# Performance work log

Hardware: AMD Instinct MI355X
Metric: run time of the kernel (lower is better)

Reference implementation:

```python
import jax, jax.numpy as jnp
import numpy as np

B, T, D = 64, 8192, 16   # batch, time, state dim
H = 128                  # recurr_size
HID = (256, 256)         # MLP hidden sizes
OUT = 1                  # output_dim
F = D + 1                # features + weight channel


def setup_inputs() -> dict:
    key = jax.random.key(0)
    ks = jax.random.split(key, 12)
    s = lambda k, shp: jax.random.normal(k, shp, jnp.float32) * 0.05
    return {
        "particles": jax.random.normal(ks[0], (B, T, D), jnp.float32),
        "weights": jax.random.uniform(ks[1], (B, T), jnp.float32),
        # GRU params: packed [r|z|n] gates; input dense has no bias (flax GRUCell),
        # hidden dense has bias.
        "Wi": s(ks[2], (F, 3 * H)),
        "Wh": s(ks[3], (H, 3 * H)),
        "bh": jnp.zeros((3 * H,), jnp.float32),
        # MLP decoder params
        "W1": s(ks[4], (H, HID[0])), "b1": jnp.zeros((HID[0],), jnp.float32),
        "W2": s(ks[5], (HID[0], HID[1])), "b2": jnp.zeros((HID[1],), jnp.float32),
        "W3": s(ks[6], (HID[1], OUT)), "b3": jnp.zeros((OUT,), jnp.float32),
        # log_std param, initialized with ones (init_log_std default)
        "log_std": jnp.ones((OUT,), jnp.float32),
    }


def _gru_last(inputs, Wi, Wh, bh):
    """Run GRU over time (axis 1 of [B,T,F]); return final hidden state [B,H].
    Equivalent to taking encoding at the last timestep."""
    h0 = jnp.zeros((inputs.shape[0], H), inputs.dtype)

    def step(h, x_t):  # x_t: [B,F]
        gi = x_t @ Wi              # [B,3H], no input bias (flax GRUCell)
        gh = h @ Wh + bh           # [B,3H]
        ir, iz, inn = jnp.split(gi, 3, axis=-1)
        hr, hz, hn = jnp.split(gh, 3, axis=-1)
        r = jax.nn.sigmoid(ir + hr)
        z = jax.nn.sigmoid(iz + hz)
        n = jnp.tanh(inn + r * hn)
        h_new = (1.0 - z) * n + z * h
        return h_new, None

    xs = jnp.swapaxes(inputs, 0, 1)  # [T,B,F]
    h_last, _ = jax.lax.scan(step, h0, xs)
    return h_last


def reference(particles, weights, Wi, Wh, bh, W1, b1, W2, b2, W3, b3, log_std):
    features = particles  # feature_fn = identity
    inputs = jnp.concatenate([features, weights[..., None]], axis=-1)  # [B,T,F]
    enc = _gru_last(inputs, Wi, Wh, bh)  # [B,H] == encoding at last timestep
    x = jax.nn.relu(enc @ W1 + b1)
    x = jax.nn.relu(x @ W2 + b2)
    mean = x @ W3 + b3  # [B,OUT]
    return mean, log_std
```

## Files before the change

kernel.cpp:

```cpp
#include <hip/hip_runtime.h>
#include <hip/hip_bf16.h>

#define B 64
#define T 8192
#define D 16
#define H 128
#define F 17
#define NTHREADS 512

typedef _Float16 half_t;
typedef _Float16 f16x8 __attribute__((ext_vector_type(8)));
typedef float f32x4 __attribute__((ext_vector_type(4)));

#define MFMA(a, b, c) __builtin_amdgcn_mfma_f32_16x16x32_f16((a), (b), (c), 0, 0, 0)

__device__ __forceinline__ float fast_rcp(float x) {
#if __has_builtin(__builtin_amdgcn_rcpf)
  return __builtin_amdgcn_rcpf(x);
#else
  return 1.0f / x;
#endif
}

#define GSTEP(RBUF, WBUF, tt, XV)                                          \
  do {                                                                     \
    const f16x8* hv8 = (const f16x8*)(RBUF);                               \
    f16x8 a0 = hv8[g16], a1 = hv8[4 + g16], a2 = hv8[8 + g16],             \
          a3 = hv8[12 + g16], a4 = hv8[16 + g16];                          \
    f32x4 ar = {b_r, b_r, b_r, b_r}, az = {b_z, b_z, b_z, b_z},            \
          an = {b_n, b_n, b_n, b_n}, ai = {0.f, 0.f, 0.f, 0.f};            \
    ar = MFMA(a0, wr0, ar); az = MFMA(a0, wz0, az); an = MFMA(a0, wn0, an);\
    ar = MFMA(a1, wr1, ar); az = MFMA(a1, wz1, az); an = MFMA(a1, wn1, an);\
    ar = MFMA(a2, wr2, ar); az = MFMA(a2, wz2, az); an = MFMA(a2, wn2, an);\
    ar = MFMA(a3, wr3, ar); az = MFMA(a3, wz3, az); an = MFMA(a3, wn3, an);\
    ar = MFMA(a4, wr4, ar); az = MFMA(a4, wz4, az); ai = MFMA(a4, wi4, ai);\
    float rr = fast_rcp(1.0f + __expf(-ar[0]));                            \
    float zz = fast_rcp(1.0f + __expf(-az[0]));                            \
    float pre = fmaf(rr, an[0], ai[0]);                                    \
    pre = fminf(fmaxf(pre, -15.0f), 15.0f);                                \
    float e2 = __expf(-2.0f * pre);                                        \
    float nn = (1.0f - e2) * fast_rcp(1.0f + e2);                          \
    hreg = fmaf(zz, hreg - nn, nn);                     \
    if (g16 == 0) (WBUF)[jj] = (half_t)hreg;                               \
    if (isx) { (WBUF)[H + tid] = (half_t)(XV);                             \
               XV = xload((tt) + 3 < T ? (tt) + 3 : T - 1); }              \
    __syncthreads();                                                       \
  } while (0)

__global__ __launch_bounds__(NTHREADS)
void policy_gru_kernel(const float* __restrict__ particles,
                       const float* __restrict__ weights,
                       const float* __restrict__ Wi, const float* __restrict__ Wh,
                       const float* __restrict__ bh,
                       const float* __restrict__ W1, const float* __restrict__ b1,
                       const float* __restrict__ W2, const float* __restrict__ b2,
                       const float* __restrict__ W3, const float* __restrict__ b3,
                       const float* __restrict__ log_std,
                       float* __restrict__ out)
{
  __shared__ __align__(16) half_t hbuf[2][160];
  __shared__ float sg[NTHREADS];
  __shared__ float red[8];

  const int tid = threadIdx.x;
  const int b   = blockIdx.x;
  const int l   = tid & 63;
  const int w   = tid >> 6;
  const int g16 = l >> 4;
  const int jn  = l & 15;
  const int jj  = w * 16 + jn;

  auto wload = [&](int gate, int s) -> f16x8 {
    f16x8 v;
    #pragma unroll
    for (int r = 0; r < 8; ++r) {
      const int k = s * 32 + g16 * 8 + r;
      float f = 0.0f;
      const int col = (gate == 0) ? jj : (gate == 1) ? 128 + jj : 256 + jj;
      if (gate <= 1) {
        if (k < 128) f = Wh[k * 384 + col];
        else if (k < 128 + F) f = Wi[(k - 128) * 384 + col];
      } else if (gate == 2) {
        if (k < 128) f = Wh[k * 384 + col];
      } else {
        if (k >= 128 && k < 128 + F) f = Wi[(k - 128) * 384 + col];
      }
      v[r] = (half_t)f;
    }
    return v;
  };
  const f16x8 wr0 = wload(0, 0), wr1 = wload(0, 1), wr2 = wload(0, 2),
              wr3 = wload(0, 3), wr4 = wload(0, 4);
  const f16x8 wz0 = wload(1, 0), wz1 = wload(1, 1), wz2 = wload(1, 2),
              wz3 = wload(1, 3), wz4 = wload(1, 4);
  const f16x8 wn0 = wload(2, 0), wn1 = wload(2, 1), wn2 = wload(2, 2),
              wn3 = wload(2, 3);
  const f16x8 wi4 = wload(3, 4);
  const float b_r = bh[jj], b_z = bh[128 + jj], b_n = bh[256 + jj];

  const bool isx = tid < F;
  auto xload = [&](int t) -> float {
    if (!isx) return 0.0f;
    if (tid < D) return particles[((size_t)b * T + t) * D + tid];
    return weights[(size_t)b * T + t];
  };

  if (tid < 160) { hbuf[0][tid] = (half_t)0.f; hbuf[1][tid] = (half_t)0.f; }
  float hreg = 0.0f;
  __syncthreads();
  if (isx) hbuf[0][H + tid] = (half_t)xload(0);
  float xA = xload(1);
  float xB = xload(2);
  __syncthreads();

  for (int t = 0; t < T; t += 2) {
    GSTEP(hbuf[0], hbuf[1], t, xA);
    GSTEP(hbuf[1], hbuf[0], t + 1, xB);
  }

  if (g16 == 0) sg[jj] = hreg;
  __syncthreads();

  float a1 = 0.0f;
  if (tid < 256) {
    a1 = b1[tid];
    #pragma unroll 4
    for (int k = 0; k < H; ++k) a1 = fmaf(sg[k], W1[k * 256 + tid], a1);
    a1 = fmaxf(a1, 0.0f);
    sg[256 + tid] = a1;
  }
  __syncthreads();

  float a2 = 0.0f;
  if (tid < 256) {
    a2 = b2[tid];
    #pragma unroll 4
    for (int k = 0; k < 256; ++k) a2 = fmaf(sg[256 + k], W2[k * 256 + tid], a2);
    a2 = fmaxf(a2, 0.0f);
    a2 *= W3[tid];
  }
  #pragma unroll
  for (int off = 32; off > 0; off >>= 1) a2 += __shfl_down(a2, off, 64);
  if (tid < 256 && (tid & 63) == 0) red[tid >> 6] = a2;
  __syncthreads();
  if (tid == 0) {
    out[b] = red[0] + red[1] + red[2] + red[3] + b3[0];
    if (b == 0) out[B] = log_std[0];
  }
}

extern "C" void kernel_launch(void* const* d_in, const int* in_sizes, int n_in,
                              void* d_out, int out_size, void* d_ws, size_t ws_size,
                              hipStream_t stream) {
  const float* particles = (const float*)d_in[0];
  const float* weights   = (const float*)d_in[1];
  const float* Wi      = (const float*)d_in[2];
  const float* Wh      = (const float*)d_in[3];
  const float* bh      = (const float*)d_in[4];
  const float* W1      = (const float*)d_in[5];
  const float* b1      = (const float*)d_in[6];
  const float* W2      = (const float*)d_in[7];
  const float* b2      = (const float*)d_in[8];
  const float* W3      = (const float*)d_in[9];
  const float* b3      = (const float*)d_in[10];
  const float* log_std = (const float*)d_in[11];

  policy_gru_kernel<<<dim3(B), dim3(NTHREADS), 0, stream>>>(
      particles, weights, Wi, Wh, bh, W1, b1, W2, b2, W3, b3, log_std,
      (float*)d_out);
}
```

Before: 3.179 ms.

## Batch 16 sequences per block and precompute input projections in separate kernel

Each block now runs 16 batch rows of the GRU recurrence at once, using all M rows of the 16x16 MFMA tiles instead of one. It launches 4 blocks instead of 64. When workspace allows, a separate kernel first precomputes x@Wi for every timestep into fp16 scratch, and the recurrence streams those values in with a 4-step prefetch. This drops the fifth MFMA k-slice and the input staging. The cost is far fewer active CUs on the serial critical path, four times more gate math per thread per step, and a large fp16 intermediate written to and read from global memory.

```diff
diff --git a/kernel.cpp b/kernel.cpp
--- a/kernel.cpp
+++ b/kernel.cpp
@@ -7,9 +7,14 @@
 #define H 128
 #define F 17
 #define NTHREADS 512
+#define MB 16
+#define NBLK 4
+#define LSTR 168
+#define GI_T (NBLK * 128 * 48)
 
 typedef _Float16 half_t;
 typedef _Float16 f16x8 __attribute__((ext_vector_type(8)));
+typedef _Float16 f16x4 __attribute__((ext_vector_type(4)));
 typedef float f32x4 __attribute__((ext_vector_type(4)));
 
 #define MFMA(a, b, c) __builtin_amdgcn_mfma_f32_16x16x32_f16((a), (b), (c), 0, 0, 0)
@@ -22,31 +27,44 @@
 #endif
 }
 
-#define GSTEP(RBUF, WBUF, tt, XV)                                          \
-  do {                                                                     \
-    const f16x8* hv8 = (const f16x8*)(RBUF);                               \
-    f16x8 a0 = hv8[g16], a1 = hv8[4 + g16], a2 = hv8[8 + g16],             \
-          a3 = hv8[12 + g16], a4 = hv8[16 + g16];                          \
-    f32x4 ar = {b_r, b_r, b_r, b_r}, az = {b_z, b_z, b_z, b_z},            \
-          an = {b_n, b_n, b_n, b_n}, ai = {0.f, 0.f, 0.f, 0.f};            \
-    ar = MFMA(a0, wr0, ar); az = MFMA(a0, wz0, az); an = MFMA(a0, wn0, an);\
-    ar = MFMA(a1, wr1, ar); az = MFMA(a1, wz1, az); an = MFMA(a1, wn1, an);\
-    ar = MFMA(a2, wr2, ar); az = MFMA(a2, wz2, az); an = MFMA(a2, wn2, an);\
-    ar = MFMA(a3, wr3, ar); az = MFMA(a3, wz3, az); an = MFMA(a3, wn3, an);\
-    ar = MFMA(a4, wr4, ar); az = MFMA(a4, wz4, az); ai = MFMA(a4, wi4, ai);\
-    float rr = fast_rcp(1.0f + __expf(-ar[0]));                            \
-    float zz = fast_rcp(1.0f + __expf(-az[0]));                            \
-    float pre = fmaf(rr, an[0], ai[0]);                                    \
-    pre = fminf(fmaxf(pre, -15.0f), 15.0f);                                \
-    float e2 = __expf(-2.0f * pre);                                        \
-    float nn = (1.0f - e2) * fast_rcp(1.0f + e2);                          \
-    hreg = fmaf(zz, hreg - nn, nn);                     \
-    if (g16 == 0) (WBUF)[jj] = (half_t)hreg;                               \
-    if (isx) { (WBUF)[H + tid] = (half_t)(XV);                             \
-               XV = xload((tt) + 3 < T ? (tt) + 3 : T - 1); }              \
-    __syncthreads();                                                       \
-  } while (0)
-
+struct GiR { f16x4 r, z, n; };
+
+#define AFRAG(hp, s) (*(const f16x8*)((hp) + arow * LSTR + (s) * 32 + mg * 8))
+
+__global__ __launch_bounds__(NTHREADS)
+void gi_kernel(const float* __restrict__ particles, const float* __restrict__ weights,
+               const float* __restrict__ Wi, half_t* __restrict__ gi)
+{
+  __shared__ float xs[MB][32][F];
+  __shared__ float wis[F][384];
+  const int g  = blockIdx.x & 3;
+  const int t0 = (blockIdx.x >> 2) * 32;
+  const int tid = threadIdx.x;
+
+  for (int i = tid; i < F * 384; i += NTHREADS) wis[i / 384][i % 384] = Wi[i];
+  for (int i = tid; i < MB * 32 * F; i += NTHREADS) {
+    int m = i / (32 * F), rest = i % (32 * F), t = rest / F, f = rest % F;
+    xs[m][t][f] = (f < D) ? particles[((size_t)(g * MB + m) * T + t0 + t) * D + f]
+                          : weights[(size_t)(g * MB + m) * T + t0 + t];
+  }
+  __syncthreads();
+
+  #pragma unroll 1
+  for (int k = 0; k < 12; ++k) {
+    const int e = tid + NTHREADS * k;
+    const int j = e / 48, r2 = e % 48, gate = r2 >> 4, m = r2 & 15;
+    const int col = gate * 128 + j;
+    #pragma unroll 1
+    for (int t = 0; t < 32; ++t) {
+      float s = 0.f;
+      #pragma unroll
+      for (int f = 0; f < F; ++f) s = fmaf(xs[m][t][f], wis[f][col], s);
+      gi[(size_t)(t0 + t) * GI_T + g * 6144 + e] = (half_t)s;
+    }
+  }
+}
+
+template<bool GIP>
 __global__ __launch_bounds__(NTHREADS)
 void policy_gru_kernel(const float* __restrict__ particles,
                        const float* __restrict__ weights,
@@ -56,27 +74,30 @@
                        const float* __restrict__ W2, const float* __restrict__ b2,
                        const float* __restrict__ W3, const float* __restrict__ b3,
                        const float* __restrict__ log_std,
+                       const half_t* __restrict__ gi,
                        float* __restrict__ out)
 {
-  __shared__ __align__(16) half_t hbuf[2][160];
-  __shared__ float sg[NTHREADS];
-  __shared__ float red[8];
+  __shared__ __align__(16) half_t hbuf[2][MB * LSTR];
+  __shared__ float sgH[MB * H];
+  __shared__ float sgA[MB * 256];
 
   const int tid = threadIdx.x;
-  const int b   = blockIdx.x;
+  const int b0  = blockIdx.x * MB;
   const int l   = tid & 63;
   const int w   = tid >> 6;
-  const int g16 = l >> 4;
+  const int mg  = l >> 4;
   const int jn  = l & 15;
-  const int jj  = w * 16 + jn;
+  const int arow = jn;
+  const int jcol = w * 16 + jn;
+  const int m0   = mg * 4;
 
   auto wload = [&](int gate, int s) -> f16x8 {
     f16x8 v;
     #pragma unroll
     for (int r = 0; r < 8; ++r) {
-      const int k = s * 32 + g16 * 8 + r;
+      const int k = s * 32 + mg * 8 + r;
+      const int col = (gate == 0) ? jcol : (gate == 1) ? 128 + jcol : 256 + jcol;
       float f = 0.0f;
-      const int col = (gate == 0) ? jj : (gate == 1) ? 128 + jj : 256 + jj;
       if (gate <= 1) {
         if (k < 128) f = Wh[k * 384 + col];
         else if (k < 128 + F) f = Wi[(k - 128) * 384 + col];
@@ -89,64 +110,125 @@
     }
     return v;
   };
-  const f16x8 wr0 = wload(0, 0), wr1 = wload(0, 1), wr2 = wload(0, 2),
-              wr3 = wload(0, 3), wr4 = wload(0, 4);
-  const f16x8 wz0 = wload(1, 0), wz1 = wload(1, 1), wz2 = wload(1, 2),
-              wz3 = wload(1, 3), wz4 = wload(1, 4);
-  const f16x8 wn0 = wload(2, 0), wn1 = wload(2, 1), wn2 = wload(2, 2),
-              wn3 = wload(2, 3);
-  const f16x8 wi4 = wload(3, 4);
-  const float b_r = bh[jj], b_z = bh[128 + jj], b_n = bh[256 + jj];
-
-  const bool isx = tid < F;
+  const f16x8 wr0 = wload(0,0), wr1 = wload(0,1), wr2 = wload(0,2), wr3 = wload(0,3);
+  const f16x8 wz0 = wload(1,0), wz1 = wload(1,1), wz2 = wload(1,2), wz3 = wload(1,3);
+  const f16x8 wn0 = wload(2,0), wn1 = wload(2,1), wn2 = wload(2,2), wn3 = wload(2,3);
+  f16x8 wr4 = {}, wz4 = {}, wi4 = {};
+  if (!GIP) { wr4 = wload(0,4); wz4 = wload(1,4); wi4 = wload(3,4); }
+  const float b_r = bh[jcol], b_z = bh[128 + jcol], b_n = bh[256 + jcol];
+
+  const bool isx = !GIP && (tid < MB * F);
+  const int xm = isx ? tid / F : 0, xf = isx ? tid % F : 0;
   auto xload = [&](int t) -> float {
     if (!isx) return 0.0f;
-    if (tid < D) return particles[((size_t)b * T + t) * D + tid];
-    return weights[(size_t)b * T + t];
+    if (xf < D) return particles[((size_t)(b0 + xm) * T + t) * D + xf];
+    return weights[(size_t)(b0 + xm) * T + t];
   };
 
-  if (tid < 160) { hbuf[0][tid] = (half_t)0.f; hbuf[1][tid] = (half_t)0.f; }
-  float hreg = 0.0f;
-  __syncthreads();
-  if (isx) hbuf[0][H + tid] = (half_t)xload(0);
-  float xA = xload(1);
-  float xB = xload(2);
-  __syncthreads();
-
-  for (int t = 0; t < T; t += 2) {
-    GSTEP(hbuf[0], hbuf[1], t, xA);
-    GSTEP(hbuf[1], hbuf[0], t + 1, xB);
-  }
-
-  if (g16 == 0) sg[jj] = hreg;
-  __syncthreads();
-
-  float a1 = 0.0f;
-  if (tid < 256) {
-    a1 = b1[tid];
+  const half_t* gbase = GIP ? (gi + blockIdx.x * 6144 + jcol * 48 + 4 * mg) : nullptr;
+  auto gload = [&](GiR& gu, int t) {
+    const half_t* gp = gbase + (size_t)t * GI_T;
+    gu.r = *(const f16x4*)(gp);
+    gu.z = *(const f16x4*)(gp + 16);
+    gu.n = *(const f16x4*)(gp + 32);
+  };
+
+  for (int i = tid; i < 2 * MB * LSTR; i += NTHREADS)
+    ((half_t*)hbuf)[i] = (half_t)0.f;
+  float hreg[4] = {0.f, 0.f, 0.f, 0.f};
+  __syncthreads();
+  float xA = 0, xB = 0, xC = 0, xD = 0;
+  GiR g0 = {}, g1 = {}, g2 = {}, g3 = {};
+  if (GIP) { gload(g0, 0); gload(g1, 1); gload(g2, 2); gload(g3, 3); }
+  else {
+    if (isx) hbuf[0][xm * LSTR + 128 + xf] = (half_t)xload(0);
+    xA = xload(1); xB = xload(2); xC = xload(3); xD = xload(4);
+  }
+  __syncthreads();
+
+#define GSTEP(RB, WB, GU, XV, TT)                                              \
+  do {                                                                         \
+    const half_t* hp = (RB);                                                   \
+    f16x8 a0 = AFRAG(hp,0), a1 = AFRAG(hp,1), a2 = AFRAG(hp,2), a3 = AFRAG(hp,3);\
+    f32x4 ar, az, an, ai;                                                      \
+    if constexpr (GIP) {                                                       \
+      _Pragma("unroll")                                                        \
+      for (int i = 0; i < 4; ++i) {                                            \
+        ar[i] = b_r + (float)GU.r[i]; az[i] = b_z + (float)GU.z[i];            \
+        an[i] = b_n;                  ai[i] = (float)GU.n[i];                  \
+      }                                                                        \
+      gload(GU, (TT) + 4 < T ? (TT) + 4 : T - 1);                              \
+      ar = MFMA(a0, wr0, ar); az = MFMA(a0, wz0, az); an = MFMA(a0, wn0, an);  \
+      ar = MFMA(a1, wr1, ar); az = MFMA(a1, wz1, az); an = MFMA(a1, wn1, an);  \
+      ar = MFMA(a2, wr2, ar); az = MFMA(a2, wz2, az); an = MFMA(a2, wn2, an);  \
+      ar = MFMA(a3, wr3, ar); az = MFMA(a3, wz3, az); an = MFMA(a3, wn3, an);  \
+    } else {                                                                   \
+      f16x8 a4 = AFRAG(hp, 4);                                                 \
+      _Pragma("unroll")                                                        \
+      for (int i = 0; i < 4; ++i) { ar[i] = b_r; az[i] = b_z; an[i] = b_n; ai[i] = 0.f; } \
+      ar = MFMA(a0, wr0, ar); az = MFMA(a0, wz0, az); an = MFMA(a0, wn0, an);  \
+      ar = MFMA(a1, wr1, ar); az = MFMA(a1, wz1, az); an = MFMA(a1, wn1, an);  \
+      ar = MFMA(a2, wr2, ar); az = MFMA(a2, wz2, az); an = MFMA(a2, wn2, an);  \
+      ar = MFMA(a3, wr3, ar); az = MFMA(a3, wz3, az); an = MFMA(a3, wn3, an);  \
+      ar = MFMA(a4, wr4, ar); az = MFMA(a4, wz4, az); ai = MFMA(a4, wi4, ai);  \
+    }                                                                          \
+    _Pragma("unroll")                                                          \
+    for (int i = 0; i < 4; ++i) {                                              \
+      float rr = fast_rcp(1.0f + __expf(-ar[i]));                              \
+      float zz = fast_rcp(1.0f + __expf(-az[i]));                              \
+      float pre = fmaf(rr, an[i], ai[i]);                                      \
+      pre = fminf(fmaxf(pre, -15.0f), 15.0f);                                  \
+      float e2 = __expf(-2.0f * pre);                                          \
+      float nn = (1.0f - e2) * fast_rcp(1.0f + e2);                            \
+      hreg[i] = fmaf(zz, hreg[i] - nn, nn);                                    \
+      (WB)[(m0 + i) * LSTR + jcol] = (half_t)hreg[i];                          \
+    }                                                                          \
+    if constexpr (!GIP) {                                                      \
+      if (isx) (WB)[xm * LSTR + 128 + xf] = (half_t)(XV);                      \
+      XV = xload((TT) + 5 < T ? (TT) + 5 : T - 1);                             \
+    }                                                                          \
+    __syncthreads();                                                           \
+  } while (0)
+
+  for (int t = 0; t < T; t += 4) {
+    GSTEP(hbuf[0], hbuf[1], g0, xA, t);
+    GSTEP(hbuf[1], hbuf[0], g1, xB, t + 1);
+    GSTEP(hbuf[0], hbuf[1], g2, xC, t + 2);
+    GSTEP(hbuf[1], hbuf[0], g3, xD, t + 3);
+  }
+#undef GSTEP
+
+  #pragma unroll
+  for (int i = 0; i < 4; ++i) sgH[(m0 + i) * H + jcol] = hreg[i];
+  __syncthreads();
+
+  const int mm = tid >> 5;
+  const int u0 = (tid & 31) * 8;
+  float a1v[8];
+  #pragma unroll
+  for (int u = 0; u < 8; ++u) a1v[u] = b1[u0 + u];
+  #pragma unroll 1
+  for (int k = 0; k < H; ++k) {
+    const float hv = sgH[mm * H + k];
+    #pragma unroll
+    for (int u = 0; u < 8; ++u) a1v[u] = fmaf(hv, W1[k * 256 + u0 + u], a1v[u]);
+  }
+  #pragma unroll
+  for (int u = 0; u < 8; ++u) sgA[mm * 256 + u0 + u] = fmaxf(a1v[u], 0.f);
+  __syncthreads();
+
+  float p = 0.f;
+  #pragma unroll 1
+  for (int u = 0; u < 8; ++u) {
+    float a2v = b2[u0 + u];
     #pragma unroll 4
-    for (int k = 0; k < H; ++k) a1 = fmaf(sg[k], W1[k * 256 + tid], a1);
-    a1 = fmaxf(a1, 0.0f);
-    sg[256 + tid] = a1;
-  }
-  __syncthreads();
-
-  float a2 = 0.0f;
-  if (tid < 256) {
-    a2 = b2[tid];
-    #pragma unroll 4
-    for (int k = 0; k < 256; ++k) a2 = fmaf(sg[256 + k], W2[k * 256 + tid], a2);
-    a2 = fmaxf(a2, 0.0f);
-    a2 *= W3[tid];
-  }
-  #pragma unroll
-  for (int off = 32; off > 0; off >>= 1) a2 += __shfl_down(a2, off, 64);
-  if (tid < 256 && (tid & 63) == 0) red[tid >> 6] = a2;
-  __syncthreads();
-  if (tid == 0) {
-    out[b] = red[0] + red[1] + red[2] + red[3] + b3[0];
-    if (b == 0) out[B] = log_std[0];
-  }
+    for (int k = 0; k < 256; ++k) a2v = fmaf(sgA[mm * 256 + k], W2[k * 256 + u0 + u], a2v);
+    p = fmaf(fmaxf(a2v, 0.f), W3[u0 + u], p);
+  }
+  #pragma unroll
+  for (int off = 16; off > 0; off >>= 1) p += __shfl_down(p, off, 32);
+  if ((tid & 31) == 0) out[b0 + mm] = p + b3[0];
+  if (blockIdx.x == 0 && tid == 0) out[B] = log_std[0];
 }
 
 extern "C" void kernel_launch(void* const* d_in, const int* in_sizes, int n_in,
@@ -165,7 +247,17 @@
   const float* b3      = (const float*)d_in[10];
   const float* log_std = (const float*)d_in[11];
 
-  policy_gru_kernel<<<dim3(B), dim3(NTHREADS), 0, stream>>>(
-      particles, weights, Wi, Wh, bh, W1, b1, W2, b2, W3, b3, log_std,
-      (float*)d_out);
-}
+  const size_t gi_bytes = (size_t)T * GI_T * sizeof(half_t);
+  if (ws_size >= gi_bytes) {
+    half_t* gi = (half_t*)d_ws;
+    gi_kernel<<<dim3(NBLK * (T / 32)), dim3(NTHREADS), 0, stream>>>(
+        particles, weights, Wi, gi);
+    policy_gru_kernel<true><<<dim3(NBLK), dim3(NTHREADS), 0, stream>>>(
+        particles, weights, Wi, Wh, bh, W1, b1, W2, b2, W3, b3, log_std,
+        gi, (float*)d_out);
+  } else {
+    policy_gru_kernel<false><<<dim3(NBLK), dim3(NTHREADS), 0, stream>>>(
+        particles, weights, Wi, Wh, bh, W1, b1, W2, b2, W3, b3, log_std,
+        nullptr, (float*)d_out);
+  }
+}
```

Measured after the change: 6.179 ms. +94.4%, slower.

## Compute input projection on VALU per thread and fold log2e into weights

Applied to the files above, without the earlier changes.

Removes the fifth K-slice of MFMAs, which handled the input features. Each thread now computes its own r/z/n input projection with 17 FMAs per gate in fp32. The current x vector is loaded with float4 from global memory and prefetched two steps ahead, and the gate work is interleaved with the hidden MFMAs. The log2(e) factors are prescaled into the weights so that exp2 can be used directly. This shortens the MFMA dependency chain and drops the x staging through LDS, at the cost of more registers and redundant global loads by every thread.

```diff
diff --git a/kernel.cpp b/kernel.cpp
--- a/kernel.cpp
+++ b/kernel.cpp
@@ -21,30 +21,42 @@
   return 1.0f / x;
 #endif
 }
+__device__ __forceinline__ float fast_exp2(float x) {
+#if __has_builtin(__builtin_amdgcn_exp2f)
+  return __builtin_amdgcn_exp2f(x);
+#else
+  return exp2f(x);
+#endif
+}
 
-#define GSTEP(RBUF, WBUF, tt, XV)                                          \
-  do {                                                                     \
-    const f16x8* hv8 = (const f16x8*)(RBUF);                               \
-    f16x8 a0 = hv8[g16], a1 = hv8[4 + g16], a2 = hv8[8 + g16],             \
-          a3 = hv8[12 + g16], a4 = hv8[16 + g16];                          \
-    f32x4 ar = {b_r, b_r, b_r, b_r}, az = {b_z, b_z, b_z, b_z},            \
-          an = {b_n, b_n, b_n, b_n}, ai = {0.f, 0.f, 0.f, 0.f};            \
-    ar = MFMA(a0, wr0, ar); az = MFMA(a0, wz0, az); an = MFMA(a0, wn0, an);\
-    ar = MFMA(a1, wr1, ar); az = MFMA(a1, wz1, az); an = MFMA(a1, wn1, an);\
-    ar = MFMA(a2, wr2, ar); az = MFMA(a2, wz2, az); an = MFMA(a2, wn2, an);\
-    ar = MFMA(a3, wr3, ar); az = MFMA(a3, wz3, az); an = MFMA(a3, wn3, an);\
-    ar = MFMA(a4, wr4, ar); az = MFMA(a4, wz4, az); ai = MFMA(a4, wi4, ai);\
-    float rr = fast_rcp(1.0f + __expf(-ar[0]));                            \
-    float zz = fast_rcp(1.0f + __expf(-az[0]));                            \
-    float pre = fmaf(rr, an[0], ai[0]);                                    \
-    pre = fminf(fmaxf(pre, -15.0f), 15.0f);                                \
-    float e2 = __expf(-2.0f * pre);                                        \
-    float nn = (1.0f - e2) * fast_rcp(1.0f + e2);                          \
-    hreg = fmaf(zz, hreg - nn, nn);                     \
-    if (g16 == 0) (WBUF)[jj] = (half_t)hreg;                               \
-    if (isx) { (WBUF)[H + tid] = (half_t)(XV);                             \
-               XV = xload((tt) + 3 < T ? (tt) + 3 : T - 1); }              \
-    __syncthreads();                                                       \
+struct XT { float v[F]; };
+struct GI { float r, z, n; };
+
+#define GSTEP(RB, WB, GE, XV, TT)                                            \
+  do {                                                                       \
+    const f16x8* hv = (const f16x8*)(RB);                                    \
+    f16x8 a0 = hv[mg], a1 = hv[4 + mg], a2 = hv[8 + mg], a3 = hv[12 + mg];   \
+    f32x4 ar = {GE.r, GE.r, GE.r, GE.r};                                     \
+    f32x4 az = {GE.z, GE.z, GE.z, GE.z};                                     \
+    f32x4 an = {bn, bn, bn, bn};                                             \
+    const float gin = GE.n;                                                  \
+    ar = MFMA(a0, wr0, ar); az = MFMA(a0, wz0, az); an = MFMA(a0, wn0, an);  \
+    ar = MFMA(a1, wr1, ar); az = MFMA(a1, wz1, az); an = MFMA(a1, wn1, an);  \
+    ar = MFMA(a2, wr2, ar); az = MFMA(a2, wz2, az); an = MFMA(a2, wn2, an);  \
+    ar = MFMA(a3, wr3, ar); az = MFMA(a3, wz3, az); an = MFMA(a3, wn3, an);  \
+               \
+    GE = gdot(XV);                                                           \
+    XV = xload((TT) + 4);                                                    \
+                                                 \
+    float rr = fast_rcp(1.0f + fast_exp2(-ar[0]));                           \
+    float zz = fast_rcp(1.0f + fast_exp2(-az[0]));                           \
+    float pre = fmaf(rr, an[0], gin);                                        \
+    pre = fminf(fmaxf(pre, -40.0f), 40.0f);                                  \
+    float e = fast_exp2(-pre);                                               \
+    float nn = (1.0f - e) * fast_rcp(1.0f + e);                              \
+    hreg = fmaf(zz, hreg - nn, nn);                       \
+    if (mg == 0) (WB)[jj] = (half_t)hreg;                                    \
+    __syncthreads();                                                         \
   } while (0)
 
 __global__ __launch_bounds__(NTHREADS)
@@ -58,7 +70,7 @@
                        const float* __restrict__ log_std,
                        float* __restrict__ out)
 {
-  __shared__ __align__(16) half_t hbuf[2][160];
+  __shared__ __align__(16) half_t hb[2][H];
   __shared__ float sg[NTHREADS];
   __shared__ float red[8];
 
@@ -66,59 +78,74 @@
   const int b   = blockIdx.x;
   const int l   = tid & 63;
   const int w   = tid >> 6;
-  const int g16 = l >> 4;
+  const int mg  = l >> 4;
   const int jn  = l & 15;
   const int jj  = w * 16 + jn;
 
+  const float L1 = 1.4426950408889634f;
+  const float L2 = 2.0f * L1;
+
   auto wload = [&](int gate, int s) -> f16x8 {
     f16x8 v;
+    const float sc  = (gate == 2) ? L2 : L1;
+    const int   col = gate * H + jj;
     #pragma unroll
     for (int r = 0; r < 8; ++r) {
-      const int k = s * 32 + g16 * 8 + r;
-      float f = 0.0f;
-      const int col = (gate == 0) ? jj : (gate == 1) ? 128 + jj : 256 + jj;
-      if (gate <= 1) {
-        if (k < 128) f = Wh[k * 384 + col];
-        else if (k < 128 + F) f = Wi[(k - 128) * 384 + col];
-      } else if (gate == 2) {
-        if (k < 128) f = Wh[k * 384 + col];
-      } else {
-        if (k >= 128 && k < 128 + F) f = Wi[(k - 128) * 384 + col];
-      }
-      v[r] = (half_t)f;
+      const int k = s * 32 + mg * 8 + r;
+      v[r] = (half_t)(Wh[k * 384 + col] * sc);
     }
     return v;
   };
-  const f16x8 wr0 = wload(0, 0), wr1 = wload(0, 1), wr2 = wload(0, 2),
-              wr3 = wload(0, 3), wr4 = wload(0, 4);
-  const f16x8 wz0 = wload(1, 0), wz1 = wload(1, 1), wz2 = wload(1, 2),
-              wz3 = wload(1, 3), wz4 = wload(1, 4);
-  const f16x8 wn0 = wload(2, 0), wn1 = wload(2, 1), wn2 = wload(2, 2),
-              wn3 = wload(2, 3);
-  const f16x8 wi4 = wload(3, 4);
-  const float b_r = bh[jj], b_z = bh[128 + jj], b_n = bh[256 + jj];
+  const f16x8 wr0 = wload(0,0), wr1 = wload(0,1), wr2 = wload(0,2), wr3 = wload(0,3);
+  const f16x8 wz0 = wload(1,0), wz1 = wload(1,1), wz2 = wload(1,2), wz3 = wload(1,3);
+  const f16x8 wn0 = wload(2,0), wn1 = wload(2,1), wn2 = wload(2,2), wn3 = wload(2,3);
 
-  const bool isx = tid < F;
-  auto xload = [&](int t) -> float {
-    if (!isx) return 0.0f;
-    if (tid < D) return particles[((size_t)b * T + t) * D + tid];
-    return weights[(size_t)b * T + t];
+  float wir[F], wiz[F], win[F];
+  #pragma unroll
+  for (int f = 0; f < F; ++f) {
+    wir[f] = Wi[f * 384 + jj]       * L1;
+    wiz[f] = Wi[f * 384 + 128 + jj] * L1;
+    win[f] = Wi[f * 384 + 256 + jj] * L2;
+  }
+  const float br = bh[jj] * L1, bz = bh[128 + jj] * L1, bn = bh[256 + jj] * L2;
+
+  auto xload = [&](int t) -> XT {
+    XT x;
+    const int tc = t < T ? t : T - 1;
+    const float4* p = (const float4*)(particles + ((size_t)b * T + tc) * D);
+    float4 q0 = p[0], q1 = p[1], q2 = p[2], q3 = p[3];
+    x.v[0]=q0.x; x.v[1]=q0.y; x.v[2]=q0.z; x.v[3]=q0.w;
+    x.v[4]=q1.x; x.v[5]=q1.y; x.v[6]=q1.z; x.v[7]=q1.w;
+    x.v[8]=q2.x; x.v[9]=q2.y; x.v[10]=q2.z; x.v[11]=q2.w;
+    x.v[12]=q3.x; x.v[13]=q3.y; x.v[14]=q3.z; x.v[15]=q3.w;
+    x.v[16] = weights[(size_t)b * T + tc];
+    return x;
+  };
+  auto gdot = [&](const XT& x) -> GI {
+    GI g; g.r = br; g.z = bz; g.n = 0.0f;
+    #pragma unroll
+    for (int f = 0; f < F; ++f) {
+      g.r = fmaf(x.v[f], wir[f], g.r);
+      g.z = fmaf(x.v[f], wiz[f], g.z);
+      g.n = fmaf(x.v[f], win[f], g.n);
+    }
+    return g;
   };
 
-  if (tid < 160) { hbuf[0][tid] = (half_t)0.f; hbuf[1][tid] = (half_t)0.f; }
+  if (tid < H) { hb[0][tid] = (half_t)0.f; hb[1][tid] = (half_t)0.f; }
   float hreg = 0.0f;
-  __syncthreads();
-  if (isx) hbuf[0][H + tid] = (half_t)xload(0);
-  float xA = xload(1);
-  float xB = xload(2);
+  GI g_e = gdot(xload(0));
+  GI g_o = gdot(xload(1));
+  XT xA = xload(2);
+  XT xB = xload(3);
   __syncthreads();
 
   for (int t = 0; t < T; t += 2) {
-    GSTEP(hbuf[0], hbuf[1], t, xA);
-    GSTEP(hbuf[1], hbuf[0], t + 1, xB);
+    GSTEP(hb[0], hb[1], g_e, xA, t);
+    GSTEP(hb[1], hb[0], g_o, xB, t + 1);
   }
 
-  if (g16 == 0) sg[jj] = hreg;
+  if (mg == 0) sg[jj] = hreg;
   __syncthreads();
 
   float a1 = 0.0f;
```

Result: slower. 5.479 ms (+72.4%).
